# Optimization experiments

Measured on AMD Instinct MI355X. Metric: run time of the kernel, lower is better.

The kernel has to match this reference:

```python
import jax, jax.numpy as jnp
import numpy as np

B, N, IN_F = 4, 2048, 256
H, HEAD_DIM = 8, 32  # out_features=256, concat=True -> head_dim=32
ALPHA = 0.2
MASK_VAL = -9e15


def setup_inputs() -> dict:
    key = jax.random.key(0)
    k1, k2, k3, k4 = jax.random.split(key, 4)
    x = jax.random.normal(k1, (B, N, IN_F), dtype=jnp.float32)
    adj = jax.random.randint(k2, (B, N, N), 0, 2, dtype=jnp.int32)
    # xavier_uniform for W [H, in, head_dim]: gain=1, fan_in=in, fan_out=head_dim
    limW = float(np.sqrt(6.0 / (IN_F + HEAD_DIM)))
    W = jax.random.uniform(k3, (H, IN_F, HEAD_DIM), dtype=jnp.float32, minval=-limW, maxval=limW)
    # xavier_uniform for a [H, 2*head_dim]: fan_in=2*head_dim, fan_out=H (2D tensor)
    lima = float(np.sqrt(6.0 / (H + 2 * HEAD_DIM)))
    a = jax.random.uniform(k4, (H, 2 * HEAD_DIM), dtype=jnp.float32, minval=-lima, maxval=lima)
    return {"x": x, "adj": adj, "W": W, "a": a}


def reference(x, adj, W, a):
    # x: [B, N, F], adj: [B, N, N], W: [H, F, D], a: [H, 2D]
    D = W.shape[-1]
    Wh = jnp.einsum('bnf,hfd->bhnd', x, W)                     # [B,H,N,D]
    a_src, a_dst = a[:, :D], a[:, D:]
    # additive score e_ij = a_src . Wh_i + a_dst . Wh_j (equivalent to concat+matmul)
    e_i = jnp.einsum('bhnd,hd->bhn', Wh, a_src)                # [B,H,N]
    e_j = jnp.einsum('bhnd,hd->bhn', Wh, a_dst)                # [B,H,N]
    scores = e_i[:, :, :, None] + e_j[:, :, None, :]           # [B,H,N,N]
    scores = jnp.where(scores > 0, scores, ALPHA * scores)     # LeakyReLU
    scores = jnp.where(adj[:, None, :, :] == 0, MASK_VAL, scores)
    probs = jax.nn.softmax(scores, axis=-1)                    # [B,H,N,N]
    h = jnp.einsum('bhij,bhjd->bhid', probs, Wh)               # [B,H,N,D]
    b, n = x.shape[0], x.shape[1]
    return h.transpose(0, 2, 1, 3).reshape(b, n, h.shape[1] * D)  # concat heads
```

## Files before the change

kernel.cpp:

```cpp
#include <hip/hip_runtime.h>

#define BB 4
#define NN 2048
#define INF 256
#define HH 8
#define DD 32
#define LOG2E 1.4426950408889634f

typedef __attribute__((ext_vector_type(8))) short short8;
typedef __attribute__((ext_vector_type(4))) float f32x4;
typedef __attribute__((address_space(3))) unsigned as3_u32;
typedef __attribute__((address_space(1))) const unsigned as1_u32;

__device__ __forceinline__ unsigned short bf16_rne(float v) {
    unsigned b = __float_as_uint(v);
    return (unsigned short)((b + 0x7fffu + ((b >> 16) & 1u)) >> 16);
}
__device__ __forceinline__ unsigned short bf16_rhu(float v) {
    return (unsigned short)((__float_as_uint(v) + 0x8000u) >> 16);
}

__global__ __launch_bounds__(256) void adjprep_kernel(
    const int* __restrict__ adj, const float* __restrict__ W,
    const float* __restrict__ a, unsigned* __restrict__ bitsG,
    float* __restrict__ we_g)
{
    const int bid = blockIdx.x, t = threadIdx.x;
    if (bid < 2048) {
        const int wv = t >> 6, l = t & 63;
        const int row = bid * 4 + wv;
        const int* ap = adj + (size_t)row * NN;
        int vreg[32];
        #pragma unroll
        for (int c = 0; c < 32; ++c) vreg[c] = ap[c * 64 + l];
        unsigned myw = 0;
        #pragma unroll
        for (int c = 0; c < 32; ++c) {
            unsigned long long m = __ballot(vreg[c] != 0);
            unsigned sel = (l & 1) ? (unsigned)(m >> 32) : (unsigned)m;
            myw = ((l >> 1) == c) ? sel : myw;
        }
        bitsG[(size_t)row * 64 + l] = myw;
        return;
    }
    const int k = bid - 2048;
    const int h = k & 7, sel = k >> 3;
    const float* wr = W + ((size_t)(h * INF + t)) * DD;
    const float* av = a + h * 2 * DD + sel * DD;
    float acc = 0.f;
    #pragma unroll
    for (int d = 0; d < DD; ++d) acc += wr[d] * av[d];
    we_g[k * INF + t] = acc * LOG2E;
}

__global__ __launch_bounds__(256) void prepw_kernel(
    const float* __restrict__ x, const float* __restrict__ W,
    const float* __restrict__ we_g, unsigned short* __restrict__ whT2,
    float* __restrict__ esrc, unsigned* __restrict__ ejP)
{
    __shared__ __align__(16) unsigned short smem[64 * 264 * 2];
    const int bid = blockIdx.x, t = threadIdx.x;
    const int role = bid & 1, id = bid >> 1;

    if (role == 0) {
        unsigned short* xb = smem;
        unsigned short* wb = smem + 64 * 264;
        const int hp = id & 3, tl = (id >> 2) & 31, b = id >> 7;
        const int n0 = tl * 64;

        #pragma unroll
        for (int p = 0; p < 16; ++p) {
            int flat = p * 1024 + t * 4;
            int row = flat >> 8, col = flat & 255;
            f32x4 g = *(const f32x4*)&x[((size_t)(b * NN + n0 + row)) * INF + col];
            unsigned a0 = __float_as_uint(g[0]) + 0x8000u;
            unsigned a1 = __float_as_uint(g[1]) + 0x8000u;
            unsigned a2 = __float_as_uint(g[2]) + 0x8000u;
            unsigned a3 = __float_as_uint(g[3]) + 0x8000u;
            uint2 pk;
            pk.x = __builtin_amdgcn_perm(a1, a0, 0x07060302u);
            pk.y = __builtin_amdgcn_perm(a3, a2, 0x07060302u);
            *(uint2*)&xb[row * 264 + col] = pk;
        }
        #pragma unroll
        for (int p = 0; p < 16; ++p) {
            int flat = p * 1024 + t * 4;
            int h2 = flat >> 13, rem = flat & 8191;
            int f = rem >> 5, d0 = rem & 31;
            f32x4 g = *(const f32x4*)&W[(((size_t)(hp * 2 + h2)) * INF + f) * DD + d0];
            #pragma unroll
            for (int i = 0; i < 4; ++i)
                wb[(h2 * 32 + d0 + i) * 264 + f] = bf16_rhu(g[i]);
        }
        __syncthreads();

        const int w = t >> 6, l = t & 63;
        const int ml = l & 15, q = l >> 4;
        f32x4 acc[4] = {};
        const unsigned short* apx = &xb[(w * 16 + ml) * 264 + q * 8];
        #pragma unroll
        for (int k0 = 0; k0 < INF; k0 += 32) {
            short8 A = *(const short8*)&apx[k0];
            #pragma unroll
            for (int c16 = 0; c16 < 4; ++c16) {
                short8 Bf = *(const short8*)&wb[(c16 * 16 + ml) * 264 + q * 8 + k0];
                acc[c16] = __builtin_amdgcn_mfma_f32_16x16x32_bf16(A, Bf, acc[c16], 0, 0, 0);
            }
        }
        __syncthreads();
        unsigned short* ldsC = xb;
        #pragma unroll
        for (int c16 = 0; c16 < 4; ++c16)
            #pragma unroll
            for (int r = 0; r < 4; ++r) {
                int col = c16 * 16 + ml;
                int rt  = w * 16 + q * 4 + r;
                ldsC[col * 72 + rt] = bf16_rhu(acc[c16][r]);
            }
        __syncthreads();
        #pragma unroll
        for (int p = 0; p < 2; ++p) {
            int g = p * 256 + t;
            int d = g & 31, jo = (g >> 5) & 7, h2 = g >> 8;
            short8 vv = *(const short8*)&ldsC[(h2 * 32 + d) * 72 + jo * 8];
            int bh = b * 8 + hp * 2 + h2;
            *(short8*)&whT2[(((size_t)bh * 256 + tl * 8 + jo) * 32 + d) * 8] = vv;
        }
        return;
    }

    float* xs    = (float*)smem;
    float* weld2 = (float*)smem + 16 * 260;
    const int tile = id & 127, b = id >> 7;
    const int n0 = tile * 16;

    #pragma unroll
    for (int p = 0; p < 4; ++p) {
        int flat = p * 1024 + t * 4;
        int row = flat >> 8, col = flat & 255;
        f32x4 g = *(const f32x4*)&x[((size_t)(b * NN + n0 + row)) * INF + col];
        *(f32x4*)&xs[row * 260 + col] = g;
    }
    #pragma unroll
    for (int p = 0; p < 4; ++p) {
        int flat = p * 1024 + t * 4;
        int k = flat >> 8, f = flat & 255;
        f32x4 g = *(const f32x4*)&we_g[flat];
        *(f32x4*)&weld2[(f >> 4) * 260 + k * 16 + (f & 15)] = g;
    }
    __syncthreads();

    const int row = t >> 4, cc = t & 15;
    f32x4 xv[4];
    #pragma unroll
    for (int i = 0; i < 4; ++i)
        xv[i] = *(const f32x4*)&xs[row * 260 + cc * 16 + i * 4];

    float keep = 0.f;
    #pragma unroll
    for (int k = 0; k < 16; ++k) {
        float s = 0.f;
        #pragma unroll
        for (int i = 0; i < 4; ++i) {
            f32x4 w4 = *(const f32x4*)&weld2[cc * 260 + k * 16 + i * 4];
            s += xv[i][0]*w4[0] + xv[i][1]*w4[1] + xv[i][2]*w4[2] + xv[i][3]*w4[3];
        }
        s += __shfl_xor(s, 1, 64);
        s += __shfl_xor(s, 2, 64);
        s += __shfl_xor(s, 4, 64);
        s += __shfl_xor(s, 8, 64);
        keep = (cc == k) ? s : keep;
    }
    const int n = n0 + row;
    if (cc < 8) {
        esrc[(b * 8 + cc) * NN + n] = keep;
    } else {
        float Ej  = __builtin_amdgcn_exp2f(keep);
        float Ej5 = __builtin_amdgcn_exp2f(0.2f * keep);
        ejP[(b * 8 + (cc - 8)) * NN + n] =
            ((unsigned)bf16_rne(Ej) << 16) | (unsigned)bf16_rne(Ej5);
    }
}

__global__ __launch_bounds__(256, 8) void attn_kernel(
    const unsigned short* __restrict__ whT2, const float* __restrict__ esrc,
    const unsigned* __restrict__ ejP, const unsigned* __restrict__ bitsG,
    float* __restrict__ out)
{
    __shared__ __align__(16) unsigned short whs[2][4096];
    __shared__ __align__(16) unsigned eps[2][128];
    const int t = threadIdx.x, w = t >> 6, l = t & 63;
    const int ml = l & 15, q = l >> 4;
    const int obid = blockIdx.x;
    const int bid = (obid & 7) * 128 + (obid >> 3);
    const int ig = bid & 31, h = (bid >> 5) & 7, b = bid >> 8;
    const int bh = b * HH + h;
    const int i0 = ig * 64 + w * 16;

    const float ei = esrc[bh * NN + i0 + ml];
    const float Gi = __builtin_amdgcn_exp2f(-0.8f * ei);

    const unsigned short* whb = whT2 + (size_t)bh * (256 * 256);
    const unsigned* epRow = ejP + bh * NN;
    const unsigned* mbase = bitsG + ((size_t)(b * NN + i0 + ml)) * 64;

    auto stage = [&](int c, int buf) {
        const char* g = (const char*)whb + c * 8192 + w * 2048 + l * 16;
        unsigned short* ld = &whs[buf][w * 1024];
        __builtin_amdgcn_global_load_lds((as1_u32*)g, (as3_u32*)ld, 16, 0, 0);
        __builtin_amdgcn_global_load_lds((as1_u32*)(g + 1024), (as3_u32*)(ld + 512), 16, 0, 0);
        if (w == 0) {
            const unsigned* g1 = epRow + c * 128 + l;
            __builtin_amdgcn_global_load_lds((as1_u32*)g1, (as3_u32*)&eps[buf][0], 4, 0, 0);
            const unsigned* g2 = g1 + 64;
            __builtin_amdgcn_global_load_lds((as1_u32*)g2, (as3_u32*)&eps[buf][64], 4, 0, 0);
        }
    };

    const short8 ones = {0x3F80, 0x3F80, 0x3F80, 0x3F80,
                         0x3F80, 0x3F80, 0x3F80, 0x3F80};
    f32x4 accP = {}, accQ = {}, accD = {};

    stage(0, 0);
    uint4 mrow = *(const uint4*)&mbase[0];
    for (int c = 0; c < 16; ++c) {
        __syncthreads();
        if (c < 15) stage(c + 1, (c + 1) & 1);
        const int buf = c & 1;
        const uint4 mcur = mrow;
        if (c < 15) mrow = *(const uint4*)&mbase[(c + 1) * 4];
        const unsigned mw[4] = {mcur.x, mcur.y, mcur.z, mcur.w};
        #pragma unroll
        for (int k = 0; k < 4; ++k) {
            const unsigned short* wp = &whs[buf][(k * 4 + q) * 256];
            short8 B0 = *(const short8*)&wp[ml * 8];
            short8 B1 = *(const short8*)&wp[(16 + ml) * 8];
            uint4 epA = *(const uint4*)&eps[buf][k * 32 + q * 8];
            uint4 epB = *(const uint4*)&eps[buf][k * 32 + q * 8 + 4];
            unsigned st = mw[k] >> (q * 8);
            union { unsigned u[4]; short8 s; } f0;
            const unsigned* ea = &epA.x;
            const unsigned* eb = &epB.x;
            #pragma unroll
            for (int pp = 0; pp < 4; ++pp) {
                unsigned pkA = (pp < 2) ? ea[2 * pp]     : eb[2 * pp - 4];
                unsigned pkB = (pp < 2) ? ea[2 * pp + 1] : eb[2 * pp - 3];
                float EjA = __uint_as_float(pkA & 0xffff0000u);
                float FjA = __uint_as_float(pkA << 16);
                float EjB = __uint_as_float(pkB & 0xffff0000u);
                float FjB = __uint_as_float(pkB << 16);
                unsigned mA = (unsigned)__builtin_amdgcn_sbfe(st, 2 * pp, 1);
                unsigned mB = (unsigned)__builtin_amdgcn_sbfe(st, 2 * pp + 1, 1);
                float pA = fmaxf(EjA, FjA * Gi);
                float pB = fmaxf(EjB, FjB * Gi);
                f0.u[pp] = __builtin_amdgcn_perm(__float_as_uint(pB) & mB,
                                                 __float_as_uint(pA) & mA,
                                                 0x07060302u);
            }
            accP = __builtin_amdgcn_mfma_f32_16x16x32_bf16(f0.s, B0, accP, 0, 0, 0);
            accQ = __builtin_amdgcn_mfma_f32_16x16x32_bf16(f0.s, B1, accQ, 0, 0, 0);
            accD = __builtin_amdgcn_mfma_f32_16x16x32_bf16(f0.s, ones, accD, 0, 0, 0);
        }
    }

    #pragma unroll
    for (int r = 0; r < 4; ++r) {
        int ir = i0 + q * 4 + r;
        float inv = 1.0f / accD[r];
        size_t ba = ((size_t)(b * NN + ir)) * (HH * DD) + h * DD;
        out[ba + ml]      = accP[r] * inv;
        out[ba + 16 + ml] = accQ[r] * inv;
    }
}

extern "C" void kernel_launch(void* const* d_in, const int* in_sizes, int n_in,
                              void* d_out, int out_size, void* d_ws, size_t ws_size,
                              hipStream_t stream) {
    (void)in_sizes; (void)n_in; (void)out_size; (void)ws_size;
    const float* x   = (const float*)d_in[0];
    const int*   adj = (const int*)d_in[1];
    const float* W   = (const float*)d_in[2];
    const float* a   = (const float*)d_in[3];
    float* out = (float*)d_out;

    char* ws = (char*)d_ws;
    unsigned short* whT2 = (unsigned short*)ws;
    float*    esrc  = (float*)(ws + (4u << 20));
    unsigned* ejP   = (unsigned*)(ws + (4u << 20) + (256u << 10));
    unsigned* bitsG = (unsigned*)(ws + (4u << 20) + (512u << 10));
    float*    we_g  = (float*)(ws + (4u << 20) + (512u << 10) + (2u << 20));

    adjprep_kernel<<<dim3(2064), dim3(256), 0, stream>>>(adj, W, a, bitsG, we_g);
    prepw_kernel  <<<dim3(1024), dim3(256), 0, stream>>>(x, W, we_g, whT2, esrc, ejP);
    attn_kernel   <<<dim3(1024), dim3(256), 0, stream>>>(whT2, esrc, ejP, bitsG, out);
}
```

Measured before the change: 151.7 us.

## Split attention key range across two wave groups and combine partials in LDS

Doubles the attn_kernel block to 512 threads. Each group of four waves handles half of the j (key) range, so each wave runs 8 iterations instead of 16. The second group writes its partial numerator and denominator accumulators to LDS, and the first group adds them before normalizing and storing. This roughly halves per-wave serial latency and adds parallelism per block. In exchange it doubles shared memory per block, adds an LDS reduction with two extra barriers, and may lower how many blocks fit on each CU.

```diff
diff --git a/kernel.cpp b/kernel.cpp
--- a/kernel.cpp
+++ b/kernel.cpp
@@ -182,38 +182,38 @@
     }
 }
 
-__global__ __launch_bounds__(256, 8) void attn_kernel(
+__global__ __launch_bounds__(512, 8) void attn_kernel(
     const unsigned short* __restrict__ whT2, const float* __restrict__ esrc,
     const unsigned* __restrict__ ejP, const unsigned* __restrict__ bitsG,
     float* __restrict__ out)
 {
-    __shared__ __align__(16) unsigned short whs[2][4096];
-    __shared__ __align__(16) unsigned eps[2][128];
+    __shared__ __align__(16) unsigned short whs[2][2][4096];
+    __shared__ __align__(16) unsigned eps[2][2][128];
     const int t = threadIdx.x, w = t >> 6, l = t & 63;
+    const int rw = w & 3, js = w >> 2;
     const int ml = l & 15, q = l >> 4;
     const int obid = blockIdx.x;
     const int bid = (obid & 7) * 128 + (obid >> 3);
     const int ig = bid & 31, h = (bid >> 5) & 7, b = bid >> 8;
     const int bh = b * HH + h;
-    const int i0 = ig * 64 + w * 16;
+    const int i0 = ig * 64 + rw * 16;
 
     const float ei = esrc[bh * NN + i0 + ml];
     const float Gi = __builtin_amdgcn_exp2f(-0.8f * ei);
 
     const unsigned short* whb = whT2 + (size_t)bh * (256 * 256);
     const unsigned* epRow = ejP + bh * NN;
-    const unsigned* mbase = bitsG + ((size_t)(b * NN + i0 + ml)) * 64;
-
-    auto stage = [&](int c, int buf) {
-        const char* g = (const char*)whb + c * 8192 + w * 2048 + l * 16;
-        unsigned short* ld = &whs[buf][w * 1024];
+    const unsigned* mbase = bitsG + ((size_t)(b * NN + i0 + ml)) * 64 + js * 32;
+
+    auto stage = [&](int it, int buf) {
+        const char* g = (const char*)whb + (js * 8 + it) * 8192 + rw * 2048 + l * 16;
+        unsigned short* ld = &whs[buf][js][rw * 1024];
         __builtin_amdgcn_global_load_lds((as1_u32*)g, (as3_u32*)ld, 16, 0, 0);
         __builtin_amdgcn_global_load_lds((as1_u32*)(g + 1024), (as3_u32*)(ld + 512), 16, 0, 0);
-        if (w == 0) {
-            const unsigned* g1 = epRow + c * 128 + l;
-            __builtin_amdgcn_global_load_lds((as1_u32*)g1, (as3_u32*)&eps[buf][0], 4, 0, 0);
-            const unsigned* g2 = g1 + 64;
-            __builtin_amdgcn_global_load_lds((as1_u32*)g2, (as3_u32*)&eps[buf][64], 4, 0, 0);
+        if (rw == 0) {
+            const unsigned* g1 = epRow + (js * 8 + it) * 128 + l;
+            __builtin_amdgcn_global_load_lds((as1_u32*)g1, (as3_u32*)&eps[buf][js][0], 4, 0, 0);
+            __builtin_amdgcn_global_load_lds((as1_u32*)(g1 + 64), (as3_u32*)&eps[buf][js][64], 4, 0, 0);
         }
     };
 
@@ -223,20 +223,20 @@
 
     stage(0, 0);
     uint4 mrow = *(const uint4*)&mbase[0];
-    for (int c = 0; c < 16; ++c) {
+    for (int it = 0; it < 8; ++it) {
         __syncthreads();
-        if (c < 15) stage(c + 1, (c + 1) & 1);
-        const int buf = c & 1;
+        if (it < 7) stage(it + 1, (it + 1) & 1);
+        const int buf = it & 1;
         const uint4 mcur = mrow;
-        if (c < 15) mrow = *(const uint4*)&mbase[(c + 1) * 4];
+        if (it < 7) mrow = *(const uint4*)&mbase[(it + 1) * 4];
         const unsigned mw[4] = {mcur.x, mcur.y, mcur.z, mcur.w};
         #pragma unroll
         for (int k = 0; k < 4; ++k) {
-            const unsigned short* wp = &whs[buf][(k * 4 + q) * 256];
+            const unsigned short* wp = &whs[buf][js][(k * 4 + q) * 256];
             short8 B0 = *(const short8*)&wp[ml * 8];
             short8 B1 = *(const short8*)&wp[(16 + ml) * 8];
-            uint4 epA = *(const uint4*)&eps[buf][k * 32 + q * 8];
-            uint4 epB = *(const uint4*)&eps[buf][k * 32 + q * 8 + 4];
+            uint4 epA = *(const uint4*)&eps[buf][js][k * 32 + q * 8];
+            uint4 epB = *(const uint4*)&eps[buf][js][k * 32 + q * 8 + 4];
             unsigned st = mw[k] >> (q * 8);
             union { unsigned u[4]; short8 s; } f0;
             const unsigned* ea = &epA.x;
@@ -263,13 +263,27 @@
         }
     }
 
-    #pragma unroll
-    for (int r = 0; r < 4; ++r) {
-        int ir = i0 + q * 4 + r;
-        float inv = 1.0f / accD[r];
-        size_t ba = ((size_t)(b * NN + ir)) * (HH * DD) + h * DD;
-        out[ba + ml]      = accP[r] * inv;
-        out[ba + 16 + ml] = accQ[r] * inv;
+    __syncthreads();
+    float* cmb = (float*)&whs[0][0][0];
+    float* myc = &cmb[(rw * 64 + l) * 13];
+    if (js == 1) {
+        *(f32x4*)&myc[0] = accP;
+        *(f32x4*)&myc[4] = accQ;
+        *(f32x4*)&myc[8] = accD;
+    }
+    __syncthreads();
+    if (js == 0) {
+        f32x4 oP = *(const f32x4*)&myc[0];
+        f32x4 oQ = *(const f32x4*)&myc[4];
+        f32x4 oD = *(const f32x4*)&myc[8];
+        #pragma unroll
+        for (int r = 0; r < 4; ++r) {
+            int ir = i0 + q * 4 + r;
+            float inv = 1.0f / (accD[r] + oD[r]);
+            size_t ba = ((size_t)(b * NN + ir)) * (HH * DD) + h * DD;
+            out[ba + ml]      = (accP[r] + oP[r]) * inv;
+            out[ba + 16 + ml] = (accQ[r] + oQ[r]) * inv;
+        }
     }
 }
 
@@ -292,5 +306,5 @@
 
     adjprep_kernel<<<dim3(2064), dim3(256), 0, stream>>>(adj, W, a, bitsG, we_g);
     prepw_kernel  <<<dim3(1024), dim3(256), 0, stream>>>(x, W, we_g, whT2, esrc, ejP);
-    attn_kernel   <<<dim3(1024), dim3(256), 0, stream>>>(whT2, esrc, ejP, bitsG, out);
-}
+    attn_kernel   <<<dim3(1024), dim3(512), 0, stream>>>(whT2, esrc, ejP, bitsG, out);
+}
```

New measurement: 153.4 us. No clear change (+1.1%).
